# Optimization experiments

Measured on AMD Instinct MI355X. Metric: run time of the kernel, lower is better.

## Reference

```python
import jax, jax.numpy as jnp
import numpy as np

N = 50000
E = 800000
G = 256          # number of graphs in the batch
F_IN = 128
H1, D1 = 12, 32  # conv1: heads, out-per-head (concat -> 384)
H2, D2 = 1, 64   # conv2: single head
NEG_SLOPE = 0.2


def setup_inputs() -> dict:
    key = jax.random.key(0)
    ks = jax.random.split(key, 12)
    x = jax.random.normal(ks[0], (N, F_IN), dtype=jnp.float32)
    edge_index = jax.random.randint(ks[1], (2, E), 0, N, dtype=jnp.int64)
    batch = jnp.sort(jax.random.randint(ks[2], (N,), 0, G, dtype=jnp.int64))
    # conv1 params (Glorot-ish scaling)
    W1 = jax.random.normal(ks[3], (F_IN, H1 * D1), dtype=jnp.float32) * (1.0 / np.sqrt(F_IN))
    att_src1 = jax.random.normal(ks[4], (H1, D1), dtype=jnp.float32) * (1.0 / np.sqrt(D1))
    att_dst1 = jax.random.normal(ks[5], (H1, D1), dtype=jnp.float32) * (1.0 / np.sqrt(D1))
    bias1 = jnp.zeros((H1 * D1,), dtype=jnp.float32)
    # conv2 params
    W2 = jax.random.normal(ks[6], (H1 * D1, H2 * D2), dtype=jnp.float32) * (1.0 / np.sqrt(H1 * D1))
    att_src2 = jax.random.normal(ks[7], (H2, D2), dtype=jnp.float32) * (1.0 / np.sqrt(D2))
    att_dst2 = jax.random.normal(ks[8], (H2, D2), dtype=jnp.float32) * (1.0 / np.sqrt(D2))
    bias2 = jnp.zeros((H2 * D2,), dtype=jnp.float32)
    return {"x": x, "edge_index": edge_index, "batch": batch,
            "W1": W1, "att_src1": att_src1, "att_dst1": att_dst1, "bias1": bias1,
            "W2": W2, "att_src2": att_src2, "att_dst2": att_dst2, "bias2": bias2}


def gat_conv(x, src, dst, W, att_src, att_dst, bias, heads, d_out):
    # x: [N, F] -> h: [N, heads, d_out]
    h = (x @ W).reshape(N, heads, d_out)
    # per-node attention halves: [N, heads]
    a_src = jnp.einsum('nhd,hd->nh', h, att_src)
    a_dst = jnp.einsum('nhd,hd->nh', h, att_dst)
    # per-edge logits (edges include self-loops): [Etot, heads]
    e = jax.nn.leaky_relu(a_src[src] + a_dst[dst], NEG_SLOPE)
    # segment softmax over incoming edges of each destination node
    m = jax.ops.segment_max(e, dst, num_segments=N)          # [N, heads]
    e = jnp.exp(e - m[dst])
    s = jax.ops.segment_sum(e, dst, num_segments=N)          # [N, heads]
    alpha = e / s[dst]
    # weighted aggregation: [N, heads, d_out]
    out = jax.ops.segment_sum(alpha[:, :, None] * h[src], dst, num_segments=N)
    return out.reshape(N, heads * d_out) + bias


def reference(x, edge_index, batch, W1, att_src1, att_dst1, bias1,
              W2, att_src2, att_dst2, bias2):
    # add self-loops (PyG GATConv default add_self_loops=True)
    loops = jnp.arange(N, dtype=edge_index.dtype)
    src = jnp.concatenate([edge_index[0], loops])
    dst = jnp.concatenate([edge_index[1], loops])

    h = jax.nn.relu(gat_conv(x, src, dst, W1, att_src1, att_dst1, bias1, H1, D1))
    h = gat_conv(h, src, dst, W2, att_src2, att_dst2, bias2, H2, D2)

    # global mean pool over graphs
    sums = jax.ops.segment_sum(h, batch, num_segments=G)                 # [G, 64]
    cnts = jax.ops.segment_sum(jnp.ones((N,), h.dtype), batch, num_segments=G)
    return sums / jnp.maximum(cnts, 1.0)[:, None]
```

## Files before the change

### kernel.cpp

```cpp
#include <hip/hip_runtime.h>

#define N_NODES 50000
#define N_EDGES 800000
#define ETOT (N_EDGES + N_NODES)
#define G_GRAPHS 256
#define F_IN 128
#define H1 12
#define D1 32
#define C1 (H1*D1)
#define C2 64
#define NEG 0.2f
#define SCAN_B 1024
#define NBLK_SCAN ((N_NODES + SCAN_B - 1)/SCAN_B)

using bf16x8  = __attribute__((ext_vector_type(8))) short;
using ushort8 = __attribute__((ext_vector_type(8))) unsigned short;
using f32x4   = __attribute__((ext_vector_type(4))) float;

__device__ __forceinline__ float lrelu(float x){ return x > 0.f ? x : NEG*x; }
__device__ __forceinline__ unsigned short f2bf(float f){
  unsigned u = __float_as_uint(f);
  u += 0x7fffu + ((u >> 16) & 1u);
  return (unsigned short)(u >> 16);
}
__device__ __forceinline__ float bf2f(unsigned short h){
  return __uint_as_float(((unsigned)h) << 16);
}
__device__ __forceinline__ float wexp(float l){ return __expf(fminf(l, 30.f)); }

#define B_CAST ((N_NODES*F_IN/4 + 255)/256)
#define B_W1   ((F_IN*C1 + 255)/256)
#define B_W2   ((C1*C2 + 255)/256)
#define B_WAB  ((32*F_IN + 255)/256)
__global__ void prep_kernel(const float* __restrict__ x, const float* __restrict__ W1,
    const float* __restrict__ W2, const float* __restrict__ att_src,
    const float* __restrict__ att_dst, unsigned short* __restrict__ xb,
    unsigned short* __restrict__ w1t, unsigned short* __restrict__ w2t,
    unsigned short* __restrict__ wAb){
  int b = blockIdx.x, tid = threadIdx.x;
  if (b < B_CAST){
    int base = (b*256 + tid)*4;
    if (base >= N_NODES*F_IN) return;
    float4 v = *(const float4*)(x + base);
    ushort4 o; o.x=f2bf(v.x); o.y=f2bf(v.y); o.z=f2bf(v.z); o.w=f2bf(v.w);
    *(ushort4*)(xb + base) = o;
  } else if (b < B_CAST + B_W1){
    int i = (b - B_CAST)*256 + tid;
    if (i >= F_IN*C1) return;
    int n = i / F_IN, k = i % F_IN;
    w1t[i] = f2bf(W1[(size_t)k*C1 + n]);
  } else if (b < B_CAST + B_W1 + B_W2){
    int i = (b - B_CAST - B_W1)*256 + tid;
    if (i >= C1*C2) return;
    int n = i / C1, k = i % C1;
    w2t[i] = f2bf(W2[(size_t)k*C2 + n]);
  } else {
    int i = (b - B_CAST - B_W1 - B_W2)*256 + tid;
    if (i >= 32*F_IN) return;
    int c = i >> 7, k = i & 127;
    float v = 0.f;
    if (c < 12){
      #pragma unroll
      for (int dd=0; dd<D1; ++dd) v += W1[(size_t)k*C1 + c*D1 + dd] * att_src[c*D1 + dd];
    } else if (c < 24){
      int h = c - 12;
      #pragma unroll
      for (int dd=0; dd<D1; ++dd) v += W1[(size_t)k*C1 + h*D1 + dd] * att_dst[h*D1 + dd];
    }
    wAb[i] = f2bf(v);
  }
}

template<int BM,int BN,int WM,int WN,bool F32OUT>
__global__ __launch_bounds__(256) void gemm_mfma(const unsigned short* __restrict__ A,
    const unsigned short* __restrict__ Bt, void* __restrict__ Cv,
    int M, int N, int K){
  constexpr int BK = 32;
  __shared__ unsigned short As2[4][BM][8];
  __shared__ unsigned short Bs2[4][BN][8];
  const int tid  = threadIdx.x;
  const int wid  = tid >> 6, lane = tid & 63;
  constexpr int NWX = BN / WN;
  const int wrow = (wid / NWX) * WM, wcol = (wid % NWX) * WN;
  constexpr int MR = WM/16, NR = WN/16;
  const int row0 = blockIdx.x * BM, col0 = blockIdx.y * BN;
  const int r = lane & 15, koct = lane >> 4;
  f32x4 acc[MR][NR];
  #pragma unroll
  for (int m=0;m<MR;m++)
    #pragma unroll
    for (int n=0;n<NR;n++) acc[m][n] = f32x4{0.f,0.f,0.f,0.f};

  for (int k0 = 0; k0 < K; k0 += BK){
    for (int s = tid; s < BM*8; s += 256){
      int rr = s >> 3, cc = (s & 7) * 4;
      int gr = row0 + rr;
      ushort4 v = (gr < M) ? *(const ushort4*)(A + (size_t)gr*K + k0 + cc)
                           : ushort4{0,0,0,0};
      *(ushort4*)(&As2[cc>>3][rr][cc&7]) = v;
    }
    for (int s = tid; s < BN*8; s += 256){
      int rr = s >> 3, cc = (s & 7) * 4;
      ushort4 v = *(const ushort4*)(Bt + (size_t)(col0+rr)*K + k0 + cc);
      *(ushort4*)(&Bs2[cc>>3][rr][cc&7]) = v;
    }
    __syncthreads();
    bf16x8 af[MR], bq[NR];
    #pragma unroll
    for (int m=0;m<MR;m++) af[m] = *(const bf16x8*)(&As2[koct][wrow + m*16 + r][0]);
    #pragma unroll
    for (int n=0;n<NR;n++) bq[n] = *(const bf16x8*)(&Bs2[koct][wcol + n*16 + r][0]);
    #pragma unroll
    for (int m=0;m<MR;m++)
      #pragma unroll
      for (int n=0;n<NR;n++)
        acc[m][n] = __builtin_amdgcn_mfma_f32_16x16x32_bf16(af[m], bq[n], acc[m][n], 0,0,0);
    __syncthreads();
  }
  #pragma unroll
  for (int m=0;m<MR;m++){
    #pragma unroll
    for (int rr=0; rr<4; rr++){
      int grow = row0 + wrow + m*16 + koct*4 + rr;
      if (grow < M){
        #pragma unroll
        for (int n=0;n<NR;n++){
          if constexpr (F32OUT)
            ((float*)Cv)[(size_t)grow*N + col0 + wcol + n*16 + r] = acc[m][n][rr];
          else
            ((unsigned short*)Cv)[(size_t)grow*N + col0 + wcol + n*16 + r] = f2bf(acc[m][n][rr]);
        }
      }
    }
  }
}

#define EGRID ((ETOT + 255)/256)
#define NGRID ((N_NODES + 255)/256)
__global__ void count_cnt_kernel(const int* __restrict__ ei, const int* __restrict__ batch,
                                 int* __restrict__ counts, int* __restrict__ cnt){
  if ((int)blockIdx.x < EGRID){
    int e = blockIdx.x*256 + threadIdx.x;
    if (e >= ETOT) return;
    int d = (e < N_EDGES) ? ei[N_EDGES + e] : (e - N_EDGES);
    atomicAdd(&counts[d], 1);
  } else {
    int n = (blockIdx.x - EGRID)*256 + threadIdx.x;
    if (n < N_NODES) atomicAdd(&cnt[batch[n]], 1);
  }
}
__global__ __launch_bounds__(SCAN_B) void scan_pass1(const int* __restrict__ counts,
    int* __restrict__ excl, int* __restrict__ bsum){
  __shared__ int sdata[SCAN_B];
  int i = blockIdx.x*SCAN_B + threadIdx.x;
  int v = (i < N_NODES) ? counts[i] : 0;
  sdata[threadIdx.x] = v;
  __syncthreads();
  for (int off=1; off<SCAN_B; off<<=1){
    int t = (threadIdx.x >= off) ? sdata[threadIdx.x-off] : 0;
    __syncthreads();
    sdata[threadIdx.x] += t;
    __syncthreads();
  }
  if (i < N_NODES) excl[i] = sdata[threadIdx.x] - v;
  if (threadIdx.x == SCAN_B-1) bsum[blockIdx.x] = sdata[SCAN_B-1];
}
__global__ void scan_pass3(int* __restrict__ rowptr, const int* __restrict__ bsum,
                           int* __restrict__ cursor){
  __shared__ int carry_s;
  int sblk = blockIdx.x >> 2;
  if (threadIdx.x == 0){
    int c = 0;
    for (int b=0; b<sblk; ++b) c += bsum[b];
    carry_s = c;
  }
  __syncthreads();
  int i = blockIdx.x*256 + (int)threadIdx.x;
  if (i < N_NODES){
    int r = rowptr[i] + carry_s;
    rowptr[i] = r; cursor[i] = r;
  }
  if (i == N_NODES) rowptr[N_NODES] = ETOT;
}
__global__ void scatter_kernel(const int* __restrict__ ei, int* __restrict__ cursor,
                               int* __restrict__ csr_src){
  int e = blockIdx.x*blockDim.x + threadIdx.x;
  if (e >= ETOT) return;
  int s, d;
  if (e < N_EDGES){ s = ei[e]; d = ei[N_EDGES + e]; } else { s = d = e - N_EDGES; }
  int slot = atomicAdd(&cursor[d], 1);
  csr_src[slot] = s;
}

__global__ __launch_bounds__(512) void agg1s_kernel(const int* __restrict__ rowptr,
    const int* __restrict__ csr, const unsigned short* __restrict__ xb,
    const float* __restrict__ asd, const unsigned short* __restrict__ w1t,
    const float* __restrict__ bias, unsigned short* __restrict__ out1){
  constexpr int ROWE = 6*F_IN + 8;
  constexpr int WROW = 32*12 + 4;
  __shared__ unsigned short agg[16*ROWE];
  __shared__ float wlds[16][WROW];

  const int tid    = threadIdx.x;
  const int slot   = tid >> 5;
  const int lane32 = tid & 31;
  const int h16    = lane32 >> 4;
  const int t16    = lane32 & 15;
  const int gbase  = tid & 32;
  const int d      = blockIdx.x*16 + slot;
  const int r0 = rowptr[d], r1 = rowptr[d+1];

  float4 ad0 = *(const float4*)(asd + (size_t)d*32 + 12);
  float4 ad1 = *(const float4*)(asd + (size_t)d*32 + 16);
  float4 ad2 = *(const float4*)(asd + (size_t)d*32 + 20);
  float ad[12] = {ad0.x,ad0.y,ad0.z,ad0.w, ad1.x,ad1.y,ad1.z,ad1.w, ad2.x,ad2.y,ad2.z,ad2.w};

  float acc[6][8];
  #pragma unroll
  for (int h=0;h<6;h++)
    #pragma unroll
    for (int i=0;i<8;i++) acc[h][i] = 0.f;
  float ss[12];
  #pragma unroll
  for (int h=0;h<12;h++) ss[h] = 0.f;

  for (int c0 = r0; c0 < r1; c0 += 32){
    int nc = min(32, r1 - c0);
    int s_st = 0;
    if (lane32 < nc){
      int j = c0 + lane32;
      s_st = csr[j];
      float4 s0 = *(const float4*)(asd + (size_t)s_st*32);
      float4 s1 = *(const float4*)(asd + (size_t)s_st*32 + 4);
      float4 s2 = *(const float4*)(asd + (size_t)s_st*32 + 8);
      float as[12] = {s0.x,s0.y,s0.z,s0.w, s1.x,s1.y,s1.z,s1.w, s2.x,s2.y,s2.z,s2.w};
      float w[12];
      #pragma unroll
      for (int h=0;h<12;h++){ w[h] = wexp(lrelu(as[h] + ad[h])); ss[h] += w[h]; }
      *(float4*)(&wlds[slot][lane32*12 + 0]) = float4{w[0],w[1],w[2],w[3]};
      *(float4*)(&wlds[slot][lane32*12 + 4]) = float4{w[4],w[5],w[6],w[7]};
      *(float4*)(&wlds[slot][lane32*12 + 8]) = float4{w[8],w[9],w[10],w[11]};
    }
    __builtin_amdgcn_wave_barrier();
    int sA = __shfl(s_st, gbase + 0);
    ushort8 xA = *(const ushort8*)(xb + (size_t)sA*F_IN + t16*8);
    ushort8 xB = {0,0,0,0,0,0,0,0};
    if (nc > 1){
      int sB = __shfl(s_st, gbase + 1);
      xB = *(const ushort8*)(xb + (size_t)sB*F_IN + t16*8);
    }
    for (int e = 0; e < nc; ++e){
      ushort8 cx = xA;
      xA = xB;
      if (e + 2 < nc){
        int sN = __shfl(s_st, gbase + e + 2);
        xB = *(const ushort8*)(xb + (size_t)sN*F_IN + t16*8);
      }
      float2 w0 = *(const float2*)(&wlds[slot][e*12 + h16*6 + 0]);
      float2 w1 = *(const float2*)(&wlds[slot][e*12 + h16*6 + 2]);
      float2 w2 = *(const float2*)(&wlds[slot][e*12 + h16*6 + 4]);
      float xf[8];
      #pragma unroll
      for (int i=0;i<8;i++) xf[i] = bf2f((unsigned short)cx[i]);
      float wv6[6] = {w0.x,w0.y, w1.x,w1.y, w2.x,w2.y};
      #pragma unroll
      for (int h=0;h<6;h++)
        #pragma unroll
        for (int i=0;i<8;i++) acc[h][i] += wv6[h]*xf[i];
    }
    __builtin_amdgcn_wave_barrier();
  }

  #pragma unroll
  for (int h=0;h<12;h++){
    #pragma unroll
    for (int off=16; off; off>>=1) ss[h] += __shfl_xor(ss[h], off);
  }
  float inv[6];
  #pragma unroll
  for (int h=0;h<6;h++) inv[h] = 1.f / ss[h16*6 + h];

  const int wv = tid >> 6, wl = tid & 63;
  const int er = wl & 15, eq = wl >> 4;
  #pragma unroll
  for (int hf = 0; hf < 2; ++hf){
    __syncthreads();
    if (h16 == hf){
      #pragma unroll
      for (int h = 0; h < 6; ++h){
        ushort8 v;
        #pragma unroll
        for (int i=0;i<8;i++) v[i] = f2bf(acc[h][i]*inv[h]);
        *(ushort8*)(&agg[slot*ROWE + h*F_IN + t16*8]) = v;
      }
    }
    __syncthreads();
    for (int tt = wv; tt < 12; tt += 8){
      int h = tt >> 1, nb = tt & 1;
      int hh = hf*6 + h;
      f32x4 c = {0.f,0.f,0.f,0.f};
      #pragma unroll
      for (int kk=0; kk<4; ++kk){
        bf16x8 af = *(const bf16x8*)(&agg[er*ROWE + h*F_IN + kk*32 + eq*8]);
        bf16x8 bq = *(const bf16x8*)(w1t + (size_t)(hh*32 + nb*16 + er)*F_IN + kk*32 + eq*8);
        c = __builtin_amdgcn_mfma_f32_16x16x32_bf16(af, bq, c, 0,0,0);
      }
      int col = hh*32 + nb*16 + er;
      float bv = bias[col];
      #pragma unroll
      for (int rr=0; rr<4; ++rr){
        int od = blockIdx.x*16 + eq*4 + rr;
        out1[(size_t)od*C1 + col] = f2bf(fmaxf(c[rr] + bv, 0.f));
      }
    }
  }
}

__global__ void a2_kernel(const unsigned short* __restrict__ h2,
    const float* __restrict__ att_src, const float* __restrict__ att_dst,
    float* __restrict__ a_src, float* __restrict__ a_dst){
  int n = blockIdx.x*blockDim.x + threadIdx.x;
  if (n >= N_NODES) return;
  const unsigned short* hp = h2 + (size_t)n*C2;
  float s=0.f, d=0.f;
  #pragma unroll
  for (int k4=0;k4<16;k4++){
    ushort4 v = *(const ushort4*)(hp + k4*4);
    int b = k4*4;
    s += bf2f(v.x)*att_src[b] + bf2f(v.y)*att_src[b+1] + bf2f(v.z)*att_src[b+2] + bf2f(v.w)*att_src[b+3];
    d += bf2f(v.x)*att_dst[b] + bf2f(v.y)*att_dst[b+1] + bf2f(v.z)*att_dst[b+2] + bf2f(v.w)*att_dst[b+3];
  }
  a_src[n]=s; a_dst[n]=d;
}

__global__ __launch_bounds__(256) void agg2s_kernel(const int* __restrict__ rowptr,
    const int* __restrict__ csr, const unsigned short* __restrict__ h2,
    const float* __restrict__ asrc, const float* __restrict__ adst,
    const float* __restrict__ bias, const int* __restrict__ batch,
    float* __restrict__ pool){
  const int tid  = threadIdx.x;
  const int slot = tid >> 4;
  const int t16  = tid & 15;
  const int base = ((tid & 63) >> 4) * 16;
  const int d    = blockIdx.x*16 + slot;
  const int r0 = rowptr[d], r1 = rowptr[d+1];
  const float ad = adst[d];

  float ssp = 0.f;
  float a0=0.f, a1=0.f, a2=0.f, a3=0.f;

  for (int c0 = r0; c0 < r1; c0 += 16){
    int nc = min(16, r1 - c0);
    int s_st = 0; float w_st = 0.f;
    if (t16 < nc){
      s_st = csr[c0 + t16];
      w_st = wexp(lrelu(asrc[s_st] + ad));
      ssp += w_st;
    }
    int sA = __shfl(s_st, base + 0);
    ushort4 xA = *(const ushort4*)(h2 + (size_t)sA*C2 + t16*4);
    ushort4 xB = {0,0,0,0};
    if (nc > 1){
      int sB = __shfl(s_st, base + 1);
      xB = *(const ushort4*)(h2 + (size_t)sB*C2 + t16*4);
    }
    for (int e = 0; e < nc; ++e){
      ushort4 cx = xA;
      xA = xB;
      if (e + 2 < nc){
        int sN = __shfl(s_st, base + e + 2);
        xB = *(const ushort4*)(h2 + (size_t)sN*C2 + t16*4);
      }
      float w = __shfl(w_st, base + e);
      a0 += w*bf2f(cx.x);
      a1 += w*bf2f(cx.y);
      a2 += w*bf2f(cx.z);
      a3 += w*bf2f(cx.w);
    }
  }
  #pragma unroll
  for (int off=8; off; off>>=1) ssp += __shfl_xor(ssp, off);
  float inv = 1.f / ssp;
  int g = batch[d];
  int fb = t16*4;
  atomicAdd(&pool[g*C2 + fb+0], a0*inv + bias[fb+0]);
  atomicAdd(&pool[g*C2 + fb+1], a1*inv + bias[fb+1]);
  atomicAdd(&pool[g*C2 + fb+2], a2*inv + bias[fb+2]);
  atomicAdd(&pool[g*C2 + fb+3], a3*inv + bias[fb+3]);
}

__global__ void finalize_kernel(const float* __restrict__ sums, const int* __restrict__ cnt,
                                float* __restrict__ out){
  int i = blockIdx.x*blockDim.x + threadIdx.x;
  if (i >= G_GRAPHS*C2) return;
  int g = i >> 6;
  out[i] = sums[i] / fmaxf((float)cnt[g], 1.f);
}

extern "C" void kernel_launch(void* const* d_in, const int* in_sizes, int n_in,
                              void* d_out, int out_size, void* d_ws, size_t ws_size,
                              hipStream_t stream) {
  const float* x        = (const float*)d_in[0];
  const int*   ei       = (const int*)  d_in[1];
  const int*   batch    = (const int*)  d_in[2];
  const float* W1       = (const float*)d_in[3];
  const float* att_src1 = (const float*)d_in[4];
  const float* att_dst1 = (const float*)d_in[5];
  const float* bias1    = (const float*)d_in[6];
  const float* W2       = (const float*)d_in[7];
  const float* att_src2 = (const float*)d_in[8];
  const float* att_dst2 = (const float*)d_in[9];
  const float* bias2    = (const float*)d_in[10];
  float* out = (float*)d_out;

  char* ws = (char*)d_ws;
  size_t o = 0;
  auto alloc = [&](size_t bytes)->size_t{ size_t r=o; o=(o+bytes+255)&~(size_t)255; return r; };

  size_t xb_o     = alloc((size_t)N_NODES*F_IN*2);
  size_t w1t_o    = alloc((size_t)C1*F_IN*2);
  size_t w2t_o    = alloc((size_t)C2*C1*2);
  size_t wab_o    = alloc((size_t)32*F_IN*2);
  size_t asd_o    = alloc((size_t)N_NODES*32*4);
  size_t out1_o   = alloc((size_t)N_NODES*C1*2);
  size_t h2_o     = alloc((size_t)N_NODES*C2*2);
  size_t asrc2_o  = alloc((size_t)N_NODES*4);
  size_t adst2_o  = alloc((size_t)N_NODES*4);
  size_t zero_beg = o;
  size_t counts_o = alloc((size_t)N_NODES*4);
  size_t pool_o   = alloc((size_t)G_GRAPHS*C2*4);
  size_t cnt_o    = alloc((size_t)G_GRAPHS*4);
  size_t zero_end = o;
  size_t rowptr_o = alloc((size_t)(N_NODES+1)*4);
  size_t bsum_o   = alloc((size_t)NBLK_SCAN*4);
  size_t cursor_o = alloc((size_t)N_NODES*4);
  size_t csr_o    = alloc((size_t)ETOT*4);

  unsigned short* xb    = (unsigned short*)(ws + xb_o);
  unsigned short* w1t   = (unsigned short*)(ws + w1t_o);
  unsigned short* w2t   = (unsigned short*)(ws + w2t_o);
  unsigned short* wab   = (unsigned short*)(ws + wab_o);
  float* asd    = (float*)(ws + asd_o);
  unsigned short* out1b = (unsigned short*)(ws + out1_o);
  unsigned short* h2b   = (unsigned short*)(ws + h2_o);
  float* asrc2  = (float*)(ws + asrc2_o);
  float* adst2  = (float*)(ws + adst2_o);
  int*   counts = (int*)  (ws + counts_o);
  float* poolf  = (float*)(ws + pool_o);
  int*   cnt    = (int*)  (ws + cnt_o);
  int*   rowptr = (int*)  (ws + rowptr_o);
  int*   bsum   = (int*)  (ws + bsum_o);
  int*   cursor = (int*)  (ws + cursor_o);
  int*   csrsrc = (int*)  (ws + csr_o);

  hipMemsetAsync(ws + zero_beg, 0, zero_end - zero_beg, stream);

  const int TPB = 256;

  prep_kernel<<<B_CAST + B_W1 + B_W2 + B_WAB, TPB, 0, stream>>>(
      x, W1, W2, att_src1, att_dst1, xb, w1t, w2t, wab);

  count_cnt_kernel<<<EGRID + NGRID, TPB, 0, stream>>>(ei, batch, counts, cnt);
  scan_pass1<<<NBLK_SCAN, SCAN_B, 0, stream>>>(counts, rowptr, bsum);
  scan_pass3<<<(N_NODES + 1 + 255)/256, TPB, 0, stream>>>(rowptr, bsum, cursor);
  scatter_kernel<<<EGRID, TPB, 0, stream>>>(ei, cursor, csrsrc);

  gemm_mfma<64,32,32,16,true><<<dim3((N_NODES+63)/64, 1), 256, 0, stream>>>(xb, wab, asd, N_NODES, 32, F_IN);
  agg1s_kernel<<<N_NODES/16, 512, 0, stream>>>(rowptr, csrsrc, xb, asd, w1t, bias1, out1b);

  gemm_mfma<64,64,32,32,false><<<dim3((N_NODES+63)/64, 1), 256, 0, stream>>>(out1b, w2t, h2b, N_NODES, C2, C1);
  a2_kernel<<<(N_NODES + TPB-1)/TPB, TPB, 0, stream>>>(h2b, att_src2, att_dst2, asrc2, adst2);
  agg2s_kernel<<<(N_NODES+15)/16, TPB, 0, stream>>>(rowptr, csrsrc, h2b, asrc2, adst2, bias2, batch, poolf);

  finalize_kernel<<<(G_GRAPHS*C2 + TPB-1)/TPB, TPB, 0, stream>>>(poolf, cnt, out);
}
```

Measured before the change: 442.1 us.

## Fuse conv2 GEMM and attention-logit computation into conv1 aggregation kernel

The conv1 aggregation kernel now keeps the ReLU'd conv1 output tile in LDS and immediately multiplies it by W2 with MFMA. It also computes the conv2 per-node attention halves in-kernel, which removes the out1 global buffer, the separate conv2 GEMM and the a2 kernel. To fit this, each destination node is handled by 16 threads covering all 12 heads instead of 32 threads covering 6 heads each. The block size drops from 512 to 256 threads. This cuts global traffic and launches but roughly doubles per-thread accumulator registers (96 floats), which may hurt occupancy and the latency hiding of the gather.

Result: faster. 424.4 us (-4.0%).

```diff
diff --git a/kernel.cpp b/kernel.cpp
--- a/kernel.cpp
+++ b/kernel.cpp
@@ -192,22 +192,26 @@
   csr_src[slot] = s;
 }
 
-__global__ __launch_bounds__(512) void agg1s_kernel(const int* __restrict__ rowptr,
+__global__ __launch_bounds__(256) void agg1g_kernel(const int* __restrict__ rowptr,
     const int* __restrict__ csr, const unsigned short* __restrict__ xb,
     const float* __restrict__ asd, const unsigned short* __restrict__ w1t,
-    const float* __restrict__ bias, unsigned short* __restrict__ out1){
+    const unsigned short* __restrict__ w2t, const float* __restrict__ bias1,
+    const float* __restrict__ att_src2, const float* __restrict__ att_dst2,
+    unsigned short* __restrict__ h2, float* __restrict__ asrc2, float* __restrict__ adst2){
   constexpr int ROWE = 6*F_IN + 8;
-  constexpr int WROW = 32*12 + 4;
+  constexpr int WROW = 16*12 + 4;
+  constexpr int ROWR = 192 + 8;
   __shared__ unsigned short agg[16*ROWE];
   __shared__ float wlds[16][WROW];
 
-  const int tid    = threadIdx.x;
-  const int slot   = tid >> 5;
-  const int lane32 = tid & 31;
-  const int h16    = lane32 >> 4;
-  const int t16    = lane32 & 15;
-  const int gbase  = tid & 32;
-  const int d      = blockIdx.x*16 + slot;
+  unsigned short* reluLDS = (unsigned short*)&wlds[0][0];
+  float* red = (float*)&agg[0];
+
+  const int tid  = threadIdx.x;
+  const int slot = tid >> 4;
+  const int t16  = tid & 15;
+  const int base = ((tid & 63) >> 4) * 16;
+  const int d    = blockIdx.x*16 + slot;
   const int r0 = rowptr[d], r1 = rowptr[d+1];
 
   float4 ad0 = *(const float4*)(asd + (size_t)d*32 + 12);
@@ -215,20 +219,20 @@
   float4 ad2 = *(const float4*)(asd + (size_t)d*32 + 20);
   float ad[12] = {ad0.x,ad0.y,ad0.z,ad0.w, ad1.x,ad1.y,ad1.z,ad1.w, ad2.x,ad2.y,ad2.z,ad2.w};
 
-  float acc[6][8];
-  #pragma unroll
-  for (int h=0;h<6;h++)
+  float acc[12][8];
+  #pragma unroll
+  for (int h=0;h<12;h++)
     #pragma unroll
     for (int i=0;i<8;i++) acc[h][i] = 0.f;
   float ss[12];
   #pragma unroll
   for (int h=0;h<12;h++) ss[h] = 0.f;
 
-  for (int c0 = r0; c0 < r1; c0 += 32){
-    int nc = min(32, r1 - c0);
+  for (int c0 = r0; c0 < r1; c0 += 16){
+    int nc = min(16, r1 - c0);
     int s_st = 0;
-    if (lane32 < nc){
-      int j = c0 + lane32;
+    if (t16 < nc){
+      int j = c0 + t16;
       s_st = csr[j];
       float4 s0 = *(const float4*)(asd + (size_t)s_st*32);
       float4 s1 = *(const float4*)(asd + (size_t)s_st*32 + 4);
@@ -237,36 +241,36 @@
       float w[12];
       #pragma unroll
       for (int h=0;h<12;h++){ w[h] = wexp(lrelu(as[h] + ad[h])); ss[h] += w[h]; }
-      *(float4*)(&wlds[slot][lane32*12 + 0]) = float4{w[0],w[1],w[2],w[3]};
-      *(float4*)(&wlds[slot][lane32*12 + 4]) = float4{w[4],w[5],w[6],w[7]};
-      *(float4*)(&wlds[slot][lane32*12 + 8]) = float4{w[8],w[9],w[10],w[11]};
+      *(float4*)(&wlds[slot][t16*12 + 0]) = float4{w[0],w[1],w[2],w[3]};
+      *(float4*)(&wlds[slot][t16*12 + 4]) = float4{w[4],w[5],w[6],w[7]};
+      *(float4*)(&wlds[slot][t16*12 + 8]) = float4{w[8],w[9],w[10],w[11]};
     }
     __builtin_amdgcn_wave_barrier();
-    int sA = __shfl(s_st, gbase + 0);
+    int sA = __shfl(s_st, base + 0);
     ushort8 xA = *(const ushort8*)(xb + (size_t)sA*F_IN + t16*8);
     ushort8 xB = {0,0,0,0,0,0,0,0};
     if (nc > 1){
-      int sB = __shfl(s_st, gbase + 1);
+      int sB = __shfl(s_st, base + 1);
       xB = *(const ushort8*)(xb + (size_t)sB*F_IN + t16*8);
     }
     for (int e = 0; e < nc; ++e){
       ushort8 cx = xA;
       xA = xB;
       if (e + 2 < nc){
-        int sN = __shfl(s_st, gbase + e + 2);
+        int sN = __shfl(s_st, base + e + 2);
         xB = *(const ushort8*)(xb + (size_t)sN*F_IN + t16*8);
       }
-      float2 w0 = *(const float2*)(&wlds[slot][e*12 + h16*6 + 0]);
-      float2 w1 = *(const float2*)(&wlds[slot][e*12 + h16*6 + 2]);
-      float2 w2 = *(const float2*)(&wlds[slot][e*12 + h16*6 + 4]);
+      float4 w0 = *(const float4*)(&wlds[slot][e*12 + 0]);
+      float4 w1 = *(const float4*)(&wlds[slot][e*12 + 4]);
+      float4 w2 = *(const float4*)(&wlds[slot][e*12 + 8]);
       float xf[8];
       #pragma unroll
       for (int i=0;i<8;i++) xf[i] = bf2f((unsigned short)cx[i]);
-      float wv6[6] = {w0.x,w0.y, w1.x,w1.y, w2.x,w2.y};
-      #pragma unroll
-      for (int h=0;h<6;h++)
+      float w[12] = {w0.x,w0.y,w0.z,w0.w, w1.x,w1.y,w1.z,w1.w, w2.x,w2.y,w2.z,w2.w};
+      #pragma unroll
+      for (int h=0;h<12;h++)
         #pragma unroll
-        for (int i=0;i<8;i++) acc[h][i] += wv6[h]*xf[i];
+        for (int i=0;i<8;i++) acc[h][i] += w[h]*xf[i];
     }
     __builtin_amdgcn_wave_barrier();
   }
@@ -274,28 +278,28 @@
   #pragma unroll
   for (int h=0;h<12;h++){
     #pragma unroll
-    for (int off=16; off; off>>=1) ss[h] += __shfl_xor(ss[h], off);
-  }
-  float inv[6];
-  #pragma unroll
-  for (int h=0;h<6;h++) inv[h] = 1.f / ss[h16*6 + h];
+    for (int off=8; off; off>>=1) ss[h] += __shfl_xor(ss[h], off);
+  }
+  float inv[12];
+  #pragma unroll
+  for (int h=0;h<12;h++) inv[h] = 1.f / ss[h];
 
   const int wv = tid >> 6, wl = tid & 63;
   const int er = wl & 15, eq = wl >> 4;
+  f32x4 h2acc = {0.f,0.f,0.f,0.f};
   #pragma unroll
   for (int hf = 0; hf < 2; ++hf){
     __syncthreads();
-    if (h16 == hf){
-      #pragma unroll
-      for (int h = 0; h < 6; ++h){
-        ushort8 v;
-        #pragma unroll
-        for (int i=0;i<8;i++) v[i] = f2bf(acc[h][i]*inv[h]);
-        *(ushort8*)(&agg[slot*ROWE + h*F_IN + t16*8]) = v;
-      }
-    }
-    __syncthreads();
-    for (int tt = wv; tt < 12; tt += 8){
+    #pragma unroll
+    for (int h = 0; h < 6; ++h){
+      int hh = hf*6 + h;
+      ushort8 v;
+      #pragma unroll
+      for (int i=0;i<8;i++) v[i] = f2bf(acc[hh][i]*inv[hh]);
+      *(ushort8*)(&agg[slot*ROWE + h*F_IN + t16*8]) = v;
+    }
+    __syncthreads();
+    for (int tt = wv; tt < 12; tt += 4){
       int h = tt >> 1, nb = tt & 1;
       int hh = hf*6 + h;
       f32x4 c = {0.f,0.f,0.f,0.f};
@@ -305,32 +309,58 @@
         bf16x8 bq = *(const bf16x8*)(w1t + (size_t)(hh*32 + nb*16 + er)*F_IN + kk*32 + eq*8);
         c = __builtin_amdgcn_mfma_f32_16x16x32_bf16(af, bq, c, 0,0,0);
       }
-      int col = hh*32 + nb*16 + er;
-      float bv = bias[col];
+      int lcol = tt*16 + er;
+      float bv = bias1[hf*192 + lcol];
       #pragma unroll
       for (int rr=0; rr<4; ++rr){
-        int od = blockIdx.x*16 + eq*4 + rr;
-        out1[(size_t)od*C1 + col] = f2bf(fmaxf(c[rr] + bv, 0.f));
+        int row = eq*4 + rr;
+        reluLDS[row*ROWR + lcol] = f2bf(fmaxf(c[rr] + bv, 0.f));
       }
     }
-  }
-}
-
-__global__ void a2_kernel(const unsigned short* __restrict__ h2,
-    const float* __restrict__ att_src, const float* __restrict__ att_dst,
-    float* __restrict__ a_src, float* __restrict__ a_dst){
-  int n = blockIdx.x*blockDim.x + threadIdx.x;
-  if (n >= N_NODES) return;
-  const unsigned short* hp = h2 + (size_t)n*C2;
-  float s=0.f, d=0.f;
-  #pragma unroll
-  for (int k4=0;k4<16;k4++){
-    ushort4 v = *(const ushort4*)(hp + k4*4);
-    int b = k4*4;
-    s += bf2f(v.x)*att_src[b] + bf2f(v.y)*att_src[b+1] + bf2f(v.z)*att_src[b+2] + bf2f(v.w)*att_src[b+3];
-    d += bf2f(v.x)*att_dst[b] + bf2f(v.y)*att_dst[b+1] + bf2f(v.z)*att_dst[b+2] + bf2f(v.w)*att_dst[b+3];
-  }
-  a_src[n]=s; a_dst[n]=d;
+    __syncthreads();
+    #pragma unroll
+    for (int kk=0; kk<6; ++kk){
+      bf16x8 af = *(const bf16x8*)(&reluLDS[er*ROWR + kk*32 + eq*8]);
+      bf16x8 bq = *(const bf16x8*)(w2t + (size_t)(wv*16 + er)*C1 + hf*192 + kk*32 + eq*8);
+      h2acc = __builtin_amdgcn_mfma_f32_16x16x32_bf16(af, bq, h2acc, 0,0,0);
+    }
+  }
+  __syncthreads();
+
+  float attS = att_src2[wv*16 + er];
+  float attD = att_dst2[wv*16 + er];
+  float psum[4], pdum[4];
+  #pragma unroll
+  for (int rr=0; rr<4; ++rr){
+    int row = eq*4 + rr;
+    int gn = blockIdx.x*16 + row;
+    h2[(size_t)gn*C2 + wv*16 + er] = f2bf(h2acc[rr]);
+    psum[rr] = h2acc[rr]*attS;
+    pdum[rr] = h2acc[rr]*attD;
+  }
+  #pragma unroll
+  for (int rr=0; rr<4; ++rr){
+    #pragma unroll
+    for (int off=8; off; off>>=1){
+      psum[rr] += __shfl_xor(psum[rr], off);
+      pdum[rr] += __shfl_xor(pdum[rr], off);
+    }
+  }
+  if (er == 0){
+    #pragma unroll
+    for (int rr=0; rr<4; ++rr){
+      int row = eq*4 + rr;
+      red[(wv*16 + row)*2 + 0] = psum[rr];
+      red[(wv*16 + row)*2 + 1] = pdum[rr];
+    }
+  }
+  __syncthreads();
+  if (tid < 32){
+    int row = tid >> 1, which = tid & 1;
+    float v = red[row*2+which] + red[(16+row)*2+which] + red[(32+row)*2+which] + red[(48+row)*2+which];
+    int gn = blockIdx.x*16 + row;
+    if (which == 0) asrc2[gn] = v; else adst2[gn] = v;
+  }
 }
 
 __global__ __launch_bounds__(256) void agg2s_kernel(const int* __restrict__ rowptr,
@@ -422,7 +452,6 @@
   size_t w2t_o    = alloc((size_t)C2*C1*2);
   size_t wab_o    = alloc((size_t)32*F_IN*2);
   size_t asd_o    = alloc((size_t)N_NODES*32*4);
-  size_t out1_o   = alloc((size_t)N_NODES*C1*2);
   size_t h2_o     = alloc((size_t)N_NODES*C2*2);
   size_t asrc2_o  = alloc((size_t)N_NODES*4);
   size_t adst2_o  = alloc((size_t)N_NODES*4);
@@ -441,7 +470,6 @@
   unsigned short* w2t   = (unsigned short*)(ws + w2t_o);
   unsigned short* wab   = (unsigned short*)(ws + wab_o);
   float* asd    = (float*)(ws + asd_o);
-  unsigned short* out1b = (unsigned short*)(ws + out1_o);
   unsigned short* h2b   = (unsigned short*)(ws + h2_o);
   float* asrc2  = (float*)(ws + asrc2_o);
   float* adst2  = (float*)(ws + adst2_o);
@@ -466,10 +494,8 @@
   scatter_kernel<<<EGRID, TPB, 0, stream>>>(ei, cursor, csrsrc);
 
   gemm_mfma<64,32,32,16,true><<<dim3((N_NODES+63)/64, 1), 256, 0, stream>>>(xb, wab, asd, N_NODES, 32, F_IN);
-  agg1s_kernel<<<N_NODES/16, 512, 0, stream>>>(rowptr, csrsrc, xb, asd, w1t, bias1, out1b);
-
-  gemm_mfma<64,64,32,32,false><<<dim3((N_NODES+63)/64, 1), 256, 0, stream>>>(out1b, w2t, h2b, N_NODES, C2, C1);
-  a2_kernel<<<(N_NODES + TPB-1)/TPB, TPB, 0, stream>>>(h2b, att_src2, att_dst2, asrc2, adst2);
+  agg1g_kernel<<<N_NODES/16, 256, 0, stream>>>(rowptr, csrsrc, xb, asd, w1t, w2t,
+                                               bias1, att_src2, att_dst2, h2b, asrc2, adst2);
   agg2s_kernel<<<(N_NODES+15)/16, TPB, 0, stream>>>(rowptr, csrsrc, h2b, asrc2, adst2, bias2, batch, poolf);
 
   finalize_kernel<<<(G_GRAPHS*C2 + TPB-1)/TPB, TPB, 0, stream>>>(poolf, cnt, out);
```
